# Kernel optimization log

Measured on AMD Instinct MI355X. Metric: run time of the kernel, lower is better.

## Reference

```python
import jax, jax.numpy as jnp
import numpy as np

N_HEADS = 8

def setup_inputs() -> dict:
    key = jax.random.key(0)
    ks = jax.random.split(key, 7)
    B, S, D = 4, 2048, 512
    s = 1.0 / np.sqrt(D)
    return {
        "input_Q": jax.random.normal(ks[0], (B, S, D), jnp.float32),
        "input_K": jax.random.normal(ks[1], (B, S, D), jnp.float32),
        "input_V": jax.random.normal(ks[2], (B, S, D), jnp.float32),
        "W_Q": jax.random.normal(ks[3], (D, D), jnp.float32) * s,
        "W_K": jax.random.normal(ks[4], (D, D), jnp.float32) * s,
        "W_V": jax.random.normal(ks[5], (D, D), jnp.float32) * s,
        "W_O": jax.random.normal(ks[6], (D, D), jnp.float32) * s,
    }

def reference(input_Q, input_K, input_V, W_Q, W_K, W_V, W_O):
    B, Sq, D = input_Q.shape
    Sk = input_K.shape[1]
    H = N_HEADS
    d_k = D // H
    # torch nn.Linear(bias=False): y = x @ W.T
    def proj(x, W):
        return (x @ W.T).reshape(B, -1, H, d_k).transpose(0, 2, 1, 3)  # [B,H,S,dk]
    Q = proj(input_Q, W_Q)
    K = proj(input_K, W_K)
    V = proj(input_V, W_V)
    scale = 1.0 / jnp.sqrt(jnp.float32(d_k))
    scores = jnp.einsum("bhqd,bhkd->bhqk", Q, K) * scale  # [B,H,Sq,Sk]
    # TriangularCausalMask: mask strict upper triangle with -inf
    causal = jnp.tril(jnp.ones((Sq, Sk), dtype=bool))
    scores = jnp.where(causal[None, None], scores, -jnp.inf)
    attn = jax.nn.softmax(scores, axis=-1)
    context = jnp.einsum("bhqk,bhkd->bhqd", attn, V)
    context = context.transpose(0, 2, 1, 3).reshape(B, Sq, D)
    return context @ W_O.T
```

## Files before the change

### kernel.cpp

```cpp
#include <hip/hip_runtime.h>
#include <hip/hip_bf16.h>
#include <math.h>

#define B_  4
#define S_  2048
#define D_  512
#define H_  8
#define DK_ 64
#define M_  (B_ * S_)

using bf16   = __bf16;
using bf16x4 = __bf16 __attribute__((ext_vector_type(4)));
using bf16x8 = __bf16 __attribute__((ext_vector_type(8)));
using f32x4  = float __attribute__((ext_vector_type(4)));

#define MFMA16(a, b, c) __builtin_amdgcn_mfma_f32_16x16x32_bf16((a), (b), (c), 0, 0, 0)
#define EXP2(x) exp2f(x)

typedef __attribute__((address_space(3))) void       lds_void;
typedef const __attribute__((address_space(1))) void gbl_void;

__device__ __forceinline__ void async16(const bf16* g, bf16* lds) {
    __builtin_amdgcn_global_load_lds((gbl_void*)g, (lds_void*)lds, 16, 0, 0);
}

__device__ __forceinline__ bf16x8 ldg8(const bf16* p) {
    return *reinterpret_cast<const bf16x8*>(p);
}

__device__ __forceinline__ size_t fragbase(int g, int k0, int kk, int t) {
    return ((((size_t)(g * 8 + k0) * 2 + kk) * 4 + t) * 64) * 8;
}

__global__ __launch_bounds__(256) void cvt_all(
    const float* __restrict__ x0, const float* __restrict__ x1, const float* __restrict__ x2,
    const float* __restrict__ w0, const float* __restrict__ w1,
    const float* __restrict__ w2, const float* __restrict__ w3,
    bf16* __restrict__ dst)
{
    const int w    = blockIdx.x * 4 + (threadIdx.x >> 6);
    const int lane = threadIdx.x & 63;
    const int lg = lane >> 4, lc = lane & 15;
    const float* src;
    int c;
    size_t dbase;
    if (w < 24576) {
        const int seg = w >> 13;
        c = w & 8191;
        src = (seg == 0) ? x0 : (seg == 1) ? x1 : x2;
        dbase = (size_t)seg << 22;
    } else {
        const int jj = w - 24576;
        const int seg = jj >> 9;
        c = jj & 511;
        src = (seg == 0) ? w0 : (seg == 1) ? w1 : (seg == 2) ? w2 : w3;
        dbase = ((size_t)3 << 22) + ((size_t)seg << 18);
    }
    const int g = c >> 6, k0 = (c >> 3) & 7, kk = (c >> 2) & 1, t = c & 3;
    const size_t soff = ((size_t)(g * 64 + t * 16 + lc) << 9) + k0 * 64 + kk * 32 + lg * 8;
    f32x4 a = *reinterpret_cast<const f32x4*>(src + soff);
    f32x4 b = *reinterpret_cast<const f32x4*>(src + soff + 4);
    bf16x8 r;
    #pragma unroll
    for (int j = 0; j < 4; ++j) { r[j] = (bf16)a[j]; r[j + 4] = (bf16)b[j]; }
    *reinterpret_cast<bf16x8*>(dst + dbase + ((size_t)c << 9) + (size_t)lane * 8) = r;
}

__global__ __launch_bounds__(256) void gemm_qkv(
    const bf16* __restrict__ Xf, const bf16* __restrict__ Wf,
    bf16* __restrict__ qkv)
{
    const int bx  = blockIdx.x;
    const int xcd = bx & 7;
    const int idx = bx >> 3;
    const int mt  = xcd + 8 * (idx & 7);
    const int rest = idx >> 3;
    const int nt  = rest & 3;
    const int z   = rest >> 2;

    const bf16* Xz = Xf + (size_t)z * M_ * D_;
    const bf16* Wz = Wf + (size_t)z * D_ * D_;
    const bool vz = (z == 2);
    const bf16* A  = vz ? Xz : Wz;
    const bf16* Bm = vz ? Wz : Xz;

    const int lane = threadIdx.x & 63;
    const int wave = threadIdx.x >> 6;
    const int lc = lane & 15;
    const int lg = lane >> 4;
    const int gA = (vz ? 2 * mt : 2 * nt) + (wave >> 1);
    const int gB = (vz ? 2 * nt : 2 * mt) + (wave & 1);

    f32x4 acc[4][4] = {};

    #pragma unroll
    for (int k0 = 0; k0 < 8; ++k0) {
        #pragma unroll
        for (int kk = 0; kk < 2; ++kk) {
            bf16x8 af[4], bfm[4];
            #pragma unroll
            for (int t = 0; t < 4; ++t)
                af[t] = ldg8(A + fragbase(gA, k0, kk, t) + (size_t)lane * 8);
            #pragma unroll
            for (int t = 0; t < 4; ++t)
                bfm[t] = ldg8(Bm + fragbase(gB, k0, kk, t) + (size_t)lane * 8);
            #pragma unroll
            for (int mi = 0; mi < 4; ++mi)
                #pragma unroll
                for (int ni = 0; ni < 4; ++ni)
                    acc[mi][ni] = MFMA16(af[mi], bfm[ni], acc[mi][ni]);
        }
    }

    if (z < 2) {
        bf16* Y = qkv + (size_t)z * M_ * D_;
        const float sc = (z == 0) ? 0.125f * 1.4426950408889634f : 1.0f;
        #pragma unroll
        for (int mi = 0; mi < 4; ++mi)
            #pragma unroll
            for (int ni = 0; ni < 4; ++ni) {
                const int d = gA * 64 + mi * 16 + lg * 4;
                const int s = gB * 64 + ni * 16 + lc;
                bf16x4 v;
                #pragma unroll
                for (int r = 0; r < 4; ++r) v[r] = (bf16)(acc[mi][ni][r] * sc);
                const size_t oidx =
                    ((((size_t)(s >> 11) * H_ + (d >> 6)) * S_
                      + (s & (S_ - 1))) << 6) + (d & 63);
                *reinterpret_cast<bf16x4*>(&Y[oidx]) = v;
            }
    } else {
        bf16* Y = qkv + (size_t)2 * M_ * D_;
        #pragma unroll
        for (int mi = 0; mi < 4; ++mi)
            #pragma unroll
            for (int ni = 0; ni < 4; ++ni) {
                const int s = gA * 64 + mi * 16 + lg * 4;
                const int d = gB * 64 + ni * 16 + lc;
                bf16x4 v;
                #pragma unroll
                for (int r = 0; r < 4; ++r) v[r] = (bf16)acc[mi][ni][r];
                const size_t oidx =
                    ((((size_t)(s >> 11)) * H_ + (d >> 6)) << 17)
                    + (size_t)(d & 63) * S_ + (s & (S_ - 1));
                *reinterpret_cast<bf16x4*>(&Y[oidx]) = v;
            }
    }
}

__global__ __launch_bounds__(256) void gemm_out(
    const bf16* __restrict__ CtxF, const bf16* __restrict__ WoF,
    float* __restrict__ out)
{
    const int bx  = blockIdx.x;
    const int xcd = bx & 7;
    const int idx = bx >> 3;
    const int mt  = xcd + 8 * (idx & 15);
    const int nt  = idx >> 4;

    const int lane = threadIdx.x & 63;
    const int wave = threadIdx.x >> 6;
    const int lc = lane & 15;
    const int lg = lane >> 4;
    const int gA = 2 * nt + (wave >> 1);
    const int tA = (wave & 1) * 2;
    const int gB = mt;

    f32x4 acc[2][4] = {};

    #pragma unroll
    for (int k0 = 0; k0 < 8; ++k0) {
        #pragma unroll
        for (int kk = 0; kk < 2; ++kk) {
            bf16x8 af[2], bfm[4];
            #pragma unroll
            for (int ai = 0; ai < 2; ++ai)
                af[ai] = ldg8(WoF + fragbase(gA, k0, kk, tA + ai) + (size_t)lane * 8);
            #pragma unroll
            for (int t = 0; t < 4; ++t)
                bfm[t] = ldg8(CtxF + fragbase(gB, k0, kk, t) + (size_t)lane * 8);
            #pragma unroll
            for (int ai = 0; ai < 2; ++ai)
                #pragma unroll
                for (int ni = 0; ni < 4; ++ni)
                    acc[ai][ni] = MFMA16(af[ai], bfm[ni], acc[ai][ni]);
        }
    }

    #pragma unroll
    for (int ai = 0; ai < 2; ++ai)
        #pragma unroll
        for (int ni = 0; ni < 4; ++ni) {
            const int d = gA * 64 + (tA + ai) * 16 + lg * 4;
            const int s = gB * 64 + ni * 16 + lc;
            *reinterpret_cast<f32x4*>(&out[(size_t)s * D_ + d]) = acc[ai][ni];
        }
}

__device__ __forceinline__ bf16x8 pfrag(const f32x4 a, const f32x4 b) {
    union U4 { bf16x4 v; unsigned int u[2]; };
    U4 pa, pb;
    #pragma unroll
    for (int r = 0; r < 4; ++r) { pa.v[r] = (bf16)a[r]; pb.v[r] = (bf16)b[r]; }
    auto r0 = __builtin_amdgcn_permlane16_swap(pa.u[0], pb.u[0], false, false);
    auto r1 = __builtin_amdgcn_permlane16_swap(pa.u[1], pb.u[1], false, false);
    union U8 { unsigned int u[4]; bf16x8 v; } out;
    out.u[0] = r0[0]; out.u[1] = r1[0]; out.u[2] = r0[1]; out.u[3] = r1[1];
    return out.v;
}

__global__ __launch_bounds__(512, 4) void attn(
    const bf16* __restrict__ QKV, bf16* __restrict__ CtxF)
{
    const int bx = blockIdx.x;
    const int bh = (bx & 7) * 4 + ((bx >> 3) & 3);
    const int pi = bx >> 5;
    const int b = bh >> 3, h = bh & 7;
    const size_t plane = (size_t)S_ * DK_;
    const bf16* Q  = QKV + (size_t)bh * plane;
    const bf16* Kp = QKV + (size_t)(B_ * H_) * plane + (size_t)bh * plane;
    const bf16* Vt = QKV + 2 * (size_t)(B_ * H_) * plane + (size_t)bh * plane;

    const int lane = threadIdx.x & 63;
    const int wave = threadIdx.x >> 6;
    const int wv   = wave & 3;
    const int half = wave >> 2;
    const int lc = lane & 15;
    const int lg = lane >> 4;
    const int sg = ((lg & 1) << 1) | (lg >> 1);
    const int srow = wv * 16 + lc;
    const int mrow = wv * 16 + lc;

    __shared__ bf16 Ks[4][64 * 64];
    __shared__ bf16 Vs[4][64 * 64];

    const int lo = pi;
    const int hi = 31 - pi;
    const int myq = half ? lo : hi;

    const int qR = myq * 64 + mrow;
    bf16x8 qf0 = ldg8(Q + (size_t)qR * DK_ + lg * 8);
    bf16x8 qf1 = ldg8(Q + (size_t)qR * DK_ + 32 + lg * 8);

    f32x4 accO[4] = {};
    float li = 0.f;

    auto stage = [&](int n) {
        const int kn = n * 64;
        if (half == 0) {
            bf16* kd = Ks[n & 3];
            #pragma unroll
            for (int i = 0; i < 2; ++i) {
                const int kc = i * 4 + lg;
                async16(Kp + (size_t)(kn + srow) * DK_ + kc * 8,
                        kd + (i * 256 + wv * 64) * 8);
            }
        } else {
            bf16* vd = Vs[n & 3];
            #pragma unroll
            for (int i = 0; i < 2; ++i) {
                const int kcv = i * 4 + sg;
                async16(Vt + (size_t)srow * S_ + kn + kcv * 8,
                        vd + (i * 256 + wv * 64) * 8);
            }
        }
    };

    stage(0); stage(1); stage(2);

    for (int j = 0; j <= hi; ++j) {
        if (j + 2 <= hi)      asm volatile("s_waitcnt vmcnt(4)" ::: "memory");
        else if (j + 1 <= hi) asm volatile("s_waitcnt vmcnt(2)" ::: "memory");
        else                  asm volatile("s_waitcnt vmcnt(0)" ::: "memory");
        __builtin_amdgcn_s_barrier();
        if (j + 3 <= hi) stage(j + 3);

        if (j <= myq) {
            const bf16* ks = Ks[j & 3];
            const bf16* vs = Vs[j & 3];

            bf16x8 kf0[4], kf1[4], vf0[4], vf1[4];
            #pragma unroll
            for (int t = 0; t < 4; ++t) {
                kf0[t] = ldg8(&ks[(t * 64 + lane) * 8]);
                kf1[t] = ldg8(&ks[(256 + t * 64 + lane) * 8]);
                vf0[t] = ldg8(&vs[(t * 64 + lane) * 8]);
                vf1[t] = ldg8(&vs[(256 + t * 64 + lane) * 8]);
            }

            f32x4 st[4];
            #pragma unroll
            for (int t = 0; t < 4; ++t) {
                f32x4 zz = {};
                zz = MFMA16(kf0[t], qf0, zz);
                st[t] = MFMA16(kf1[t], qf1, zz);
            }
            float rs = 0.f;
            if (j == myq) {
                #pragma unroll
                for (int t = 0; t < 4; ++t)
                    #pragma unroll
                    for (int r = 0; r < 4; ++r) {
                        const int kl = t * 16 + lg * 4 + r;
                        const float pv = EXP2((kl <= mrow) ? st[t][r] : -1e30f);
                        st[t][r] = pv;
                        rs += pv;
                    }
            } else {
                #pragma unroll
                for (int t = 0; t < 4; ++t)
                    #pragma unroll
                    for (int r = 0; r < 4; ++r) {
                        const float pv = EXP2(st[t][r]);
                        st[t][r] = pv;
                        rs += pv;
                    }
            }
            li += rs;

            const bf16x8 p0 = pfrag(st[0], st[1]);
            const bf16x8 p1 = pfrag(st[2], st[3]);

            #pragma unroll
            for (int t = 0; t < 4; ++t) {
                accO[t] = MFMA16(vf0[t], p0, accO[t]);
                accO[t] = MFMA16(vf1[t], p1, accO[t]);
            }
        }
    }

    li += __shfl_xor(li, 16); li += __shfl_xor(li, 32);
    const float rl = 1.0f / li;
    __syncthreads();
    bf16* T = &Ks[0][0] + wave * 1280;

    #pragma unroll
    for (int t = 0; t < 4; ++t) {
        bf16x4 ov;
        #pragma unroll
        for (int r = 0; r < 4; ++r) ov[r] = (bf16)(accO[t][r] * rl);
        *reinterpret_cast<bf16x4*>(&T[lc * 72 + t * 16 + lg * 4]) = ov;
    }
    #pragma unroll
    for (int kk = 0; kk < 2; ++kk) {
        bf16x8 o8 = ldg8(&T[lc * 72 + kk * 32 + lg * 8]);
        *reinterpret_cast<bf16x8*>(
            &CtxF[fragbase(b * 32 + myq, h, kk, wv) + (size_t)lane * 8]) = o8;
    }
}

extern "C" void kernel_launch(void* const* d_in, const int* in_sizes, int n_in,
                              void* d_out, int out_size, void* d_ws, size_t ws_size,
                              hipStream_t stream)
{
    float* out = (float*)d_out;

    bf16* Xf   = (bf16*)d_ws;
    bf16* Wf   = Xf + (size_t)3 * M_ * D_;
    bf16* qkv  = Wf + (size_t)4 * D_ * D_;
    bf16* ctxF = qkv + (size_t)3 * M_ * D_;

    cvt_all<<<6656, 256, 0, stream>>>(
        (const float*)d_in[0], (const float*)d_in[1], (const float*)d_in[2],
        (const float*)d_in[3], (const float*)d_in[4], (const float*)d_in[5],
        (const float*)d_in[6], Xf);

    gemm_qkv<<<dim3(768), 256, 0, stream>>>(Xf, Wf, qkv);
    attn<<<dim3(512), 512, 0, stream>>>(qkv, ctxF);
    gemm_out<<<dim3(512), 256, 0, stream>>>(ctxF, Wf + (size_t)3 * D_ * D_, out);
}
```

Before: 174.7 us.

## Stage GEMM operand fragments through triple-buffered LDS via async global-to-LDS loads

Result: no change. 174.8 us (+0.1%).

```diff
diff --git a/kernel.cpp b/kernel.cpp
--- a/kernel.cpp
+++ b/kernel.cpp
@@ -88,28 +88,55 @@
     const int wave = threadIdx.x >> 6;
     const int lc = lane & 15;
     const int lg = lane >> 4;
-    const int gA = (vz ? 2 * mt : 2 * nt) + (wave >> 1);
-    const int gB = (vz ? 2 * nt : 2 * mt) + (wave & 1);
+    const int gAb = vz ? 2 * mt : 2 * nt;
+    const int gBb = vz ? 2 * nt : 2 * mt;
+    const int aIdx = wave >> 1;
+    const int bIdx = wave & 1;
+    const int gA = gAb + aIdx;
+    const int gB = gBb + bIdx;
+
+    __shared__ bf16 Ab[3][4096];
+    __shared__ bf16 Bb[3][4096];
+
+    auto stage = [&](int s) {
+        const int k0 = s >> 1, kk = s & 1;
+        bf16* ad = Ab[s % 3];
+        bf16* bd = Bb[s % 3];
+        #pragma unroll
+        for (int i = 0; i < 4; ++i) {
+            const int c  = wave * 4 + i;
+            const int gx = (c >> 2) & 1;
+            const int t  = c & 3;
+            const bf16* srcb = (c < 8) ? A + fragbase(gAb + gx, k0, kk, t)
+                                       : Bm + fragbase(gBb + gx, k0, kk, t);
+            bf16* dstb = ((c < 8) ? ad : bd) + (gx * 4 + t) * 512;
+            async16(srcb + (size_t)lane * 8, dstb + (size_t)lane * 8);
+        }
+    };
 
     f32x4 acc[4][4] = {};
 
-    #pragma unroll
-    for (int k0 = 0; k0 < 8; ++k0) {
-        #pragma unroll
-        for (int kk = 0; kk < 2; ++kk) {
-            bf16x8 af[4], bfm[4];
-            #pragma unroll
-            for (int t = 0; t < 4; ++t)
-                af[t] = ldg8(A + fragbase(gA, k0, kk, t) + (size_t)lane * 8);
-            #pragma unroll
-            for (int t = 0; t < 4; ++t)
-                bfm[t] = ldg8(Bm + fragbase(gB, k0, kk, t) + (size_t)lane * 8);
-            #pragma unroll
-            for (int mi = 0; mi < 4; ++mi)
-                #pragma unroll
-                for (int ni = 0; ni < 4; ++ni)
-                    acc[mi][ni] = MFMA16(af[mi], bfm[ni], acc[mi][ni]);
-        }
+    stage(0); stage(1);
+
+    for (int s = 0; s < 16; ++s) {
+        if (s + 1 < 16) asm volatile("s_waitcnt vmcnt(4)" ::: "memory");
+        else            asm volatile("s_waitcnt vmcnt(0)" ::: "memory");
+        __builtin_amdgcn_s_barrier();
+        if (s + 2 < 16) stage(s + 2);
+
+        const bf16* ab = Ab[s % 3] + aIdx * 2048;
+        const bf16* bb = Bb[s % 3] + bIdx * 2048;
+        bf16x8 af[4], bfm[4];
+        #pragma unroll
+        for (int t = 0; t < 4; ++t) {
+            af[t]  = ldg8(ab + t * 512 + (size_t)lane * 8);
+            bfm[t] = ldg8(bb + t * 512 + (size_t)lane * 8);
+        }
+        #pragma unroll
+        for (int mi = 0; mi < 4; ++mi)
+            #pragma unroll
+            for (int ni = 0; ni < 4; ++ni)
+                acc[mi][ni] = MFMA16(af[mi], bfm[ni], acc[mi][ni]);
     }
 
     if (z < 2) {
@@ -166,25 +193,52 @@
     const int tA = (wave & 1) * 2;
     const int gB = mt;
 
+    __shared__ bf16 Ab[3][4096];
+    __shared__ bf16 Bb[3][2048];
+
+    auto stage = [&](int s) {
+        const int k0 = s >> 1, kk = s & 1;
+        bf16* ad = Ab[s % 3];
+        bf16* bd = Bb[s % 3];
+        #pragma unroll
+        for (int i = 0; i < 3; ++i) {
+            const int c = wave * 3 + i;
+            if (c < 8) {
+                const int gx = c >> 2, t = c & 3;
+                async16(WoF + fragbase(2 * nt + gx, k0, kk, t) + (size_t)lane * 8,
+                        ad + (gx * 4 + t) * 512 + (size_t)lane * 8);
+            } else {
+                const int t = c - 8;
+                async16(CtxF + fragbase(gB, k0, kk, t) + (size_t)lane * 8,
+                        bd + t * 512 + (size_t)lane * 8);
+            }
+        }
+    };
+
     f32x4 acc[2][4] = {};
 
-    #pragma unroll
-    for (int k0 = 0; k0 < 8; ++k0) {
-        #pragma unroll
-        for (int kk = 0; kk < 2; ++kk) {
-            bf16x8 af[2], bfm[4];
-            #pragma unroll
-            for (int ai = 0; ai < 2; ++ai)
-                af[ai] = ldg8(WoF + fragbase(gA, k0, kk, tA + ai) + (size_t)lane * 8);
-            #pragma unroll
-            for (int t = 0; t < 4; ++t)
-                bfm[t] = ldg8(CtxF + fragbase(gB, k0, kk, t) + (size_t)lane * 8);
-            #pragma unroll
-            for (int ai = 0; ai < 2; ++ai)
-                #pragma unroll
-                for (int ni = 0; ni < 4; ++ni)
-                    acc[ai][ni] = MFMA16(af[ai], bfm[ni], acc[ai][ni]);
-        }
+    stage(0); stage(1);
+
+    for (int s = 0; s < 16; ++s) {
+        if (s + 1 < 16) asm volatile("s_waitcnt vmcnt(3)" ::: "memory");
+        else            asm volatile("s_waitcnt vmcnt(0)" ::: "memory");
+        __builtin_amdgcn_s_barrier();
+        if (s + 2 < 16) stage(s + 2);
+
+        const bf16* ab = Ab[s % 3] + (wave >> 1) * 2048;
+        const bf16* bb = Bb[s % 3];
+        bf16x8 af[2], bfm[4];
+        #pragma unroll
+        for (int ai = 0; ai < 2; ++ai)
+            af[ai] = ldg8(ab + (tA + ai) * 512 + (size_t)lane * 8);
+        #pragma unroll
+        for (int t = 0; t < 4; ++t)
+            bfm[t] = ldg8(bb + t * 512 + (size_t)lane * 8);
+        #pragma unroll
+        for (int ai = 0; ai < 2; ++ai)
+            #pragma unroll
+            for (int ni = 0; ni < 4; ++ni)
+                acc[ai][ni] = MFMA16(af[ai], bfm[ni], acc[ai][ni]);
     }
 
     #pragma unroll
```

## Fuse four kernels into two using software grid barriers

Applied to the files above, without the earlier changes.

After: 348.6 us. +99.6%, slower.

```diff
diff --git a/kernel.cpp b/kernel.cpp
--- a/kernel.cpp
+++ b/kernel.cpp
@@ -32,44 +32,72 @@
     return ((((size_t)(g * 8 + k0) * 2 + kk) * 4 + t) * 64) * 8;
 }
 
-__global__ __launch_bounds__(256) void cvt_all(
-    const float* __restrict__ x0, const float* __restrict__ x1, const float* __restrict__ x2,
-    const float* __restrict__ w0, const float* __restrict__ w1,
-    const float* __restrict__ w2, const float* __restrict__ w3,
-    bf16* __restrict__ dst)
+__device__ __forceinline__ void gridbar(unsigned long long* cnt, unsigned G) {
+    __syncthreads();
+    if (threadIdx.x == 0) {
+        __threadfence();
+        unsigned long long v = __hip_atomic_fetch_add(
+            cnt, 1ULL, __ATOMIC_ACQ_REL, __HIP_MEMORY_SCOPE_AGENT);
+        const unsigned long long target = (v / G + 1) * G;
+        while (__hip_atomic_load(cnt, __ATOMIC_ACQUIRE,
+                                 __HIP_MEMORY_SCOPE_AGENT) < target)
+            __builtin_amdgcn_s_sleep(8);
+        __threadfence();
+    }
+    __syncthreads();
+}
+
+__global__ __launch_bounds__(256, 3) void k1_cvt_qkv(
+    const float* __restrict__ x0, const float* __restrict__ x1,
+    const float* __restrict__ x2, const float* __restrict__ w0,
+    const float* __restrict__ w1, const float* __restrict__ w2,
+    const float* __restrict__ w3, bf16* __restrict__ dst,
+    bf16* __restrict__ qkv, unsigned long long* bar)
 {
-    const int w    = blockIdx.x * 4 + (threadIdx.x >> 6);
     const int lane = threadIdx.x & 63;
-    const int lg = lane >> 4, lc = lane & 15;
-    const float* src;
-    int c;
-    size_t dbase;
-    if (w < 24576) {
-        const int seg = w >> 13;
-        c = w & 8191;
-        src = (seg == 0) ? x0 : (seg == 1) ? x1 : x2;
-        dbase = (size_t)seg << 22;
-    } else {
-        const int jj = w - 24576;
-        const int seg = jj >> 9;
-        c = jj & 511;
-        src = (seg == 0) ? w0 : (seg == 1) ? w1 : (seg == 2) ? w2 : w3;
-        dbase = ((size_t)3 << 22) + ((size_t)seg << 18);
-    }
-    const int g = c >> 6, k0 = (c >> 3) & 7, kk = (c >> 2) & 1, t = c & 3;
-    const size_t soff = ((size_t)(g * 64 + t * 16 + lc) << 9) + k0 * 64 + kk * 32 + lg * 8;
-    f32x4 a = *reinterpret_cast<const f32x4*>(src + soff);
-    f32x4 b = *reinterpret_cast<const f32x4*>(src + soff + 4);
-    bf16x8 r;
-    #pragma unroll
-    for (int j = 0; j < 4; ++j) { r[j] = (bf16)a[j]; r[j + 4] = (bf16)b[j]; }
-    *reinterpret_cast<bf16x8*>(dst + dbase + ((size_t)c << 9) + (size_t)lane * 8) = r;
-}
-
-__global__ __launch_bounds__(256) void gemm_qkv(
-    const bf16* __restrict__ Xf, const bf16* __restrict__ Wf,
-    bf16* __restrict__ qkv)
-{
+    const int wv   = threadIdx.x >> 6;
+    const int lc = lane & 15;
+    const int lg = lane >> 4;
+
+    {
+        const int gw = blockIdx.x * 4 + wv;
+        #pragma unroll
+        for (int i = 0; i < 9; ++i) {
+            const int cw = gw + 3072 * i;
+            if (cw >= 26624) break;
+            const float* src;
+            int c;
+            size_t dbase;
+            if (cw < 24576) {
+                const int seg = cw >> 13;
+                c = cw & 8191;
+                src = (seg == 0) ? x0 : (seg == 1) ? x1 : x2;
+                dbase = (size_t)seg << 22;
+            } else {
+                const int jj = cw - 24576;
+                const int seg = jj >> 9;
+                c = jj & 511;
+                src = (seg == 0) ? w0 : (seg == 1) ? w1 : (seg == 2) ? w2 : w3;
+                dbase = ((size_t)3 << 22) + ((size_t)seg << 18);
+            }
+            const int g = c >> 6, k0 = (c >> 3) & 7, kk = (c >> 2) & 1, t = c & 3;
+            const size_t soff = ((size_t)(g * 64 + t * 16 + lc) << 9)
+                                + k0 * 64 + kk * 32 + lg * 8;
+            f32x4 a = *reinterpret_cast<const f32x4*>(src + soff);
+            f32x4 b = *reinterpret_cast<const f32x4*>(src + soff + 4);
+            bf16x8 r;
+            #pragma unroll
+            for (int j = 0; j < 4; ++j) { r[j] = (bf16)a[j]; r[j + 4] = (bf16)b[j]; }
+            *reinterpret_cast<bf16x8*>(dst + dbase + ((size_t)c << 9)
+                                       + (size_t)lane * 8) = r;
+        }
+    }
+
+    gridbar(bar, 768);
+
+    const bf16* Xf = dst;
+    const bf16* Wf = dst + (size_t)3 * M_ * D_;
+
     const int bx  = blockIdx.x;
     const int xcd = bx & 7;
     const int idx = bx >> 3;
@@ -84,12 +112,8 @@
     const bf16* A  = vz ? Xz : Wz;
     const bf16* Bm = vz ? Wz : Xz;
 
-    const int lane = threadIdx.x & 63;
-    const int wave = threadIdx.x >> 6;
-    const int lc = lane & 15;
-    const int lg = lane >> 4;
-    const int gA = (vz ? 2 * mt : 2 * nt) + (wave >> 1);
-    const int gB = (vz ? 2 * nt : 2 * mt) + (wave & 1);
+    const int gA = (vz ? 2 * mt : 2 * nt) + (wv >> 1);
+    const int gB = (vz ? 2 * nt : 2 * mt) + (wv & 1);
 
     f32x4 acc[4][4] = {};
 
@@ -146,55 +170,6 @@
                 *reinterpret_cast<bf16x4*>(&Y[oidx]) = v;
             }
     }
-}
-
-__global__ __launch_bounds__(256) void gemm_out(
-    const bf16* __restrict__ CtxF, const bf16* __restrict__ WoF,
-    float* __restrict__ out)
-{
-    const int bx  = blockIdx.x;
-    const int xcd = bx & 7;
-    const int idx = bx >> 3;
-    const int mt  = xcd + 8 * (idx & 15);
-    const int nt  = idx >> 4;
-
-    const int lane = threadIdx.x & 63;
-    const int wave = threadIdx.x >> 6;
-    const int lc = lane & 15;
-    const int lg = lane >> 4;
-    const int gA = 2 * nt + (wave >> 1);
-    const int tA = (wave & 1) * 2;
-    const int gB = mt;
-
-    f32x4 acc[2][4] = {};
-
-    #pragma unroll
-    for (int k0 = 0; k0 < 8; ++k0) {
-        #pragma unroll
-        for (int kk = 0; kk < 2; ++kk) {
-            bf16x8 af[2], bfm[4];
-            #pragma unroll
-            for (int ai = 0; ai < 2; ++ai)
-                af[ai] = ldg8(WoF + fragbase(gA, k0, kk, tA + ai) + (size_t)lane * 8);
-            #pragma unroll
-            for (int t = 0; t < 4; ++t)
-                bfm[t] = ldg8(CtxF + fragbase(gB, k0, kk, t) + (size_t)lane * 8);
-            #pragma unroll
-            for (int ai = 0; ai < 2; ++ai)
-                #pragma unroll
-                for (int ni = 0; ni < 4; ++ni)
-                    acc[ai][ni] = MFMA16(af[ai], bfm[ni], acc[ai][ni]);
-        }
-    }
-
-    #pragma unroll
-    for (int ai = 0; ai < 2; ++ai)
-        #pragma unroll
-        for (int ni = 0; ni < 4; ++ni) {
-            const int d = gA * 64 + (tA + ai) * 16 + lg * 4;
-            const int s = gB * 64 + ni * 16 + lc;
-            *reinterpret_cast<f32x4*>(&out[(size_t)s * D_ + d]) = acc[ai][ni];
-        }
 }
 
 __device__ __forceinline__ bf16x8 pfrag(const f32x4 a, const f32x4 b) {
@@ -209,143 +184,183 @@
     return out.v;
 }
 
-__global__ __launch_bounds__(512, 4) void attn(
-    const bf16* __restrict__ QKV, bf16* __restrict__ CtxF)
+__global__ __launch_bounds__(512, 4) void k2_attn_out(
+    const bf16* __restrict__ QKV, bf16* __restrict__ CtxF,
+    const bf16* __restrict__ WoF, float* __restrict__ out,
+    unsigned long long* bar)
 {
     const int bx = blockIdx.x;
-    const int bh = (bx & 7) * 4 + ((bx >> 3) & 3);
-    const int pi = bx >> 5;
-    const int b = bh >> 3, h = bh & 7;
-    const size_t plane = (size_t)S_ * DK_;
-    const bf16* Q  = QKV + (size_t)bh * plane;
-    const bf16* Kp = QKV + (size_t)(B_ * H_) * plane + (size_t)bh * plane;
-    const bf16* Vt = QKV + 2 * (size_t)(B_ * H_) * plane + (size_t)bh * plane;
-
     const int lane = threadIdx.x & 63;
     const int wave = threadIdx.x >> 6;
-    const int wv   = wave & 3;
-    const int half = wave >> 2;
     const int lc = lane & 15;
     const int lg = lane >> 4;
-    const int sg = ((lg & 1) << 1) | (lg >> 1);
-    const int srow = wv * 16 + lc;
-    const int mrow = wv * 16 + lc;
 
     __shared__ bf16 Ks[4][64 * 64];
     __shared__ bf16 Vs[4][64 * 64];
 
-    const int lo = pi;
-    const int hi = 31 - pi;
-    const int myq = half ? lo : hi;
-
-    const int qR = myq * 64 + mrow;
-    bf16x8 qf0 = ldg8(Q + (size_t)qR * DK_ + lg * 8);
-    bf16x8 qf1 = ldg8(Q + (size_t)qR * DK_ + 32 + lg * 8);
-
-    f32x4 accO[4] = {};
-    float li = 0.f;
-
-    auto stage = [&](int n) {
-        const int kn = n * 64;
-        if (half == 0) {
-            bf16* kd = Ks[n & 3];
-            #pragma unroll
-            for (int i = 0; i < 2; ++i) {
-                const int kc = i * 4 + lg;
-                async16(Kp + (size_t)(kn + srow) * DK_ + kc * 8,
-                        kd + (i * 256 + wv * 64) * 8);
-            }
-        } else {
-            bf16* vd = Vs[n & 3];
-            #pragma unroll
-            for (int i = 0; i < 2; ++i) {
-                const int kcv = i * 4 + sg;
-                async16(Vt + (size_t)srow * S_ + kn + kcv * 8,
-                        vd + (i * 256 + wv * 64) * 8);
-            }
-        }
-    };
-
-    stage(0); stage(1); stage(2);
-
-    for (int j = 0; j <= hi; ++j) {
-        if (j + 2 <= hi)      asm volatile("s_waitcnt vmcnt(4)" ::: "memory");
-        else if (j + 1 <= hi) asm volatile("s_waitcnt vmcnt(2)" ::: "memory");
-        else                  asm volatile("s_waitcnt vmcnt(0)" ::: "memory");
-        __builtin_amdgcn_s_barrier();
-        if (j + 3 <= hi) stage(j + 3);
-
-        if (j <= myq) {
-            const bf16* ks = Ks[j & 3];
-            const bf16* vs = Vs[j & 3];
-
-            bf16x8 kf0[4], kf1[4], vf0[4], vf1[4];
-            #pragma unroll
-            for (int t = 0; t < 4; ++t) {
-                kf0[t] = ldg8(&ks[(t * 64 + lane) * 8]);
-                kf1[t] = ldg8(&ks[(256 + t * 64 + lane) * 8]);
-                vf0[t] = ldg8(&vs[(t * 64 + lane) * 8]);
-                vf1[t] = ldg8(&vs[(256 + t * 64 + lane) * 8]);
-            }
-
-            f32x4 st[4];
-            #pragma unroll
-            for (int t = 0; t < 4; ++t) {
-                f32x4 zz = {};
-                zz = MFMA16(kf0[t], qf0, zz);
-                st[t] = MFMA16(kf1[t], qf1, zz);
-            }
-            float rs = 0.f;
-            if (j == myq) {
+    {
+        const int bh = (bx & 7) * 4 + ((bx >> 3) & 3);
+        const int pi = bx >> 5;
+        const int b = bh >> 3, h = bh & 7;
+        const size_t plane = (size_t)S_ * DK_;
+        const bf16* Q  = QKV + (size_t)bh * plane;
+        const bf16* Kp = QKV + (size_t)(B_ * H_) * plane + (size_t)bh * plane;
+        const bf16* Vt = QKV + 2 * (size_t)(B_ * H_) * plane + (size_t)bh * plane;
+
+        const int wv   = wave & 3;
+        const int half = wave >> 2;
+        const int sg = ((lg & 1) << 1) | (lg >> 1);
+        const int srow = wv * 16 + lc;
+        const int mrow = wv * 16 + lc;
+
+        const int lo = pi;
+        const int hi = 31 - pi;
+        const int myq = half ? lo : hi;
+
+        const int qR = myq * 64 + mrow;
+        bf16x8 qf0 = ldg8(Q + (size_t)qR * DK_ + lg * 8);
+        bf16x8 qf1 = ldg8(Q + (size_t)qR * DK_ + 32 + lg * 8);
+
+        f32x4 accO[4] = {};
+        float li = 0.f;
+
+        auto stage = [&](int n) {
+            const int kn = n * 64;
+            if (half == 0) {
+                bf16* kd = Ks[n & 3];
+                #pragma unroll
+                for (int i = 0; i < 2; ++i) {
+                    const int kc = i * 4 + lg;
+                    async16(Kp + (size_t)(kn + srow) * DK_ + kc * 8,
+                            kd + (i * 256 + wv * 64) * 8);
+                }
+            } else {
+                bf16* vd = Vs[n & 3];
+                #pragma unroll
+                for (int i = 0; i < 2; ++i) {
+                    const int kcv = i * 4 + sg;
+                    async16(Vt + (size_t)srow * S_ + kn + kcv * 8,
+                            vd + (i * 256 + wv * 64) * 8);
+                }
+            }
+        };
+
+        stage(0); stage(1); stage(2);
+
+        for (int j = 0; j <= hi; ++j) {
+            if (j + 2 <= hi)      asm volatile("s_waitcnt vmcnt(4)" ::: "memory");
+            else if (j + 1 <= hi) asm volatile("s_waitcnt vmcnt(2)" ::: "memory");
+            else                  asm volatile("s_waitcnt vmcnt(0)" ::: "memory");
+            __builtin_amdgcn_s_barrier();
+            if (j + 3 <= hi) stage(j + 3);
+
+            if (j <= myq) {
+                const bf16* ks = Ks[j & 3];
+                const bf16* vs = Vs[j & 3];
+
+                bf16x8 kf0[4], kf1[4], vf0[4], vf1[4];
+                #pragma unroll
+                for (int t = 0; t < 4; ++t) {
+                    kf0[t] = ldg8(&ks[(t * 64 + lane) * 8]);
+                    kf1[t] = ldg8(&ks[(256 + t * 64 + lane) * 8]);
+                    vf0[t] = ldg8(&vs[(t * 64 + lane) * 8]);
+                    vf1[t] = ldg8(&vs[(256 + t * 64 + lane) * 8]);
+                }
+
+                f32x4 st[4];
+                #pragma unroll
+                for (int t = 0; t < 4; ++t) {
+                    f32x4 zz = {};
+                    zz = MFMA16(kf0[t], qf0, zz);
+                    st[t] = MFMA16(kf1[t], qf1, zz);
+                }
+                float rs = 0.f;
+                if (j == myq) {
+                    #pragma unroll
+                    for (int t = 0; t < 4; ++t)
+                        #pragma unroll
+                        for (int r = 0; r < 4; ++r) {
+                            const int kl = t * 16 + lg * 4 + r;
+                            const float pv = EXP2((kl <= mrow) ? st[t][r] : -1e30f);
+                            st[t][r] = pv;
+                            rs += pv;
+                        }
+                } else {
+                    #pragma unroll
+                    for (int t = 0; t < 4; ++t)
+                        #pragma unroll
+                        for (int r = 0; r < 4; ++r) {
+                            const float pv = EXP2(st[t][r]);
+                            st[t][r] = pv;
+                            rs += pv;
+                        }
+                }
+                li += rs;
+
+                const bf16x8 p0 = pfrag(st[0], st[1]);
+                const bf16x8 p1 = pfrag(st[2], st[3]);
+
+                #pragma unroll
+                for (int t = 0; t < 4; ++t) {
+                    accO[t] = MFMA16(vf0[t], p0, accO[t]);
+                    accO[t] = MFMA16(vf1[t], p1, accO[t]);
+                }
+            }
+        }
+
+        li += __shfl_xor(li, 16); li += __shfl_xor(li, 32);
+        const float rl = 1.0f / li;
+        __syncthreads();
+        bf16* T = &Ks[0][0] + wave * 1280;
+
+        #pragma unroll
+        for (int t = 0; t < 4; ++t) {
+            bf16x4 ov;
+            #pragma unroll
+            for (int r = 0; r < 4; ++r) ov[r] = (bf16)(accO[t][r] * rl);
+            *reinterpret_cast<bf16x4*>(&T[lc * 72 + t * 16 + lg * 4]) = ov;
+        }
+        #pragma unroll
+        for (int kk = 0; kk < 2; ++kk) {
+            bf16x8 o8 = ldg8(&T[lc * 72 + kk * 32 + lg * 8]);
+            *reinterpret_cast<bf16x8*>(
+                &CtxF[fragbase(b * 32 + myq, h, kk, wv) + (size_t)lane * 8]) = o8;
+        }
+    }
+
+    gridbar(bar, 512);
+
+    {
+        const int xcd = bx & 7;
+        const int idx = bx >> 3;
+        const int mt  = xcd + 8 * (idx & 15);
+        const int nt  = idx >> 4;
+        const int gA = 2 * nt + (wave >> 2);
+        const int tA = wave & 3;
+
+        f32x4 acc2[4] = {};
+
+        #pragma unroll
+        for (int k0 = 0; k0 < 8; ++k0) {
+            #pragma unroll
+            for (int kk = 0; kk < 2; ++kk) {
+                bf16x8 af = ldg8(WoF + fragbase(gA, k0, kk, tA) + (size_t)lane * 8);
+                bf16x8 bfm[4];
                 #pragma unroll
                 for (int t = 0; t < 4; ++t)
-                    #pragma unroll
-                    for (int r = 0; r < 4; ++r) {
-                        const int kl = t * 16 + lg * 4 + r;
-                        const float pv = EXP2((kl <= mrow) ? st[t][r] : -1e30f);
-                        st[t][r] = pv;
-                        rs += pv;
-                    }
-            } else {
-                #pragma unroll
-                for (int t = 0; t < 4; ++t)
-                    #pragma unroll
-                    for (int r = 0; r < 4; ++r) {
-                        const float pv = EXP2(st[t][r]);
-                        st[t][r] = pv;
-                        rs += pv;
-                    }
-            }
-            li += rs;
-
-            const bf16x8 p0 = pfrag(st[0], st[1]);
-            const bf16x8 p1 = pfrag(st[2], st[3]);
-
-            #pragma unroll
-            for (int t = 0; t < 4; ++t) {
-                accO[t] = MFMA16(vf0[t], p0, accO[t]);
-                accO[t] = MFMA16(vf1[t], p1, accO[t]);
-            }
-        }
-    }
-
-    li += __shfl_xor(li, 16); li += __shfl_xor(li, 32);
-    const float rl = 1.0f / li;
-    __syncthreads();
-    bf16* T = &Ks[0][0] + wave * 1280;
-
-    #pragma unroll
-    for (int t = 0; t < 4; ++t) {
-        bf16x4 ov;
-        #pragma unroll
-        for (int r = 0; r < 4; ++r) ov[r] = (bf16)(accO[t][r] * rl);
-        *reinterpret_cast<bf16x4*>(&T[lc * 72 + t * 16 + lg * 4]) = ov;
-    }
-    #pragma unroll
-    for (int kk = 0; kk < 2; ++kk) {
-        bf16x8 o8 = ldg8(&T[lc * 72 + kk * 32 + lg * 8]);
-        *reinterpret_cast<bf16x8*>(
-            &CtxF[fragbase(b * 32 + myq, h, kk, wv) + (size_t)lane * 8]) = o8;
+                    bfm[t] = ldg8(CtxF + fragbase(mt, k0, kk, t) + (size_t)lane * 8);
+                #pragma unroll
+                for (int ni = 0; ni < 4; ++ni)
+                    acc2[ni] = MFMA16(af, bfm[ni], acc2[ni]);
+            }
+        }
+
+        #pragma unroll
+        for (int ni = 0; ni < 4; ++ni) {
+            const int d = gA * 64 + tA * 16 + lg * 4;
+            const int s = mt * 64 + ni * 16 + lc;
+            *reinterpret_cast<f32x4*>(&out[(size_t)s * D_ + d]) = acc2[ni];
+        }
     }
 }
 
@@ -355,17 +370,20 @@
 {
     float* out = (float*)d_out;
 
-    bf16* Xf   = (bf16*)d_ws;
-    bf16* Wf   = Xf + (size_t)3 * M_ * D_;
+    bf16* dst  = (bf16*)d_ws;
+    bf16* Wf   = dst + (size_t)3 * M_ * D_;
     bf16* qkv  = Wf + (size_t)4 * D_ * D_;
     bf16* ctxF = qkv + (size_t)3 * M_ * D_;
-
-    cvt_all<<<6656, 256, 0, stream>>>(
+    unsigned long long* bars =
+        (unsigned long long*)(ctxF + (size_t)M_ * D_);
+
+    hipMemsetAsync(bars, 0, 64, stream);
+
+    k1_cvt_qkv<<<dim3(768), 256, 0, stream>>>(
         (const float*)d_in[0], (const float*)d_in[1], (const float*)d_in[2],
         (const float*)d_in[3], (const float*)d_in[4], (const float*)d_in[5],
-        (const float*)d_in[6], Xf);
-
-    gemm_qkv<<<dim3(768), 256, 0, stream>>>(Xf, Wf, qkv);
-    attn<<<dim3(512), 512, 0, stream>>>(qkv, ctxF);
-    gemm_out<<<dim3(512), 256, 0, stream>>>(ctxF, Wf + (size_t)3 * D_ * D_, out);
-}
+        (const float*)d_in[6], dst, qkv, bars);
+
+    k2_attn_out<<<dim3(512), 512, 0, stream>>>(
+        qkv, ctxF, Wf + (size_t)3 * D_ * D_, out, bars + 1);
+}
```

## Split attention key tiles across wave halves instead of pairing query tiles

Applied to the files above, without the earlier changes.

Result: slower. 182.8 us (+4.6%).

```diff
diff --git a/kernel.cpp b/kernel.cpp
--- a/kernel.cpp
+++ b/kernel.cpp
@@ -214,7 +214,7 @@
 {
     const int bx = blockIdx.x;
     const int bh = (bx & 7) * 4 + ((bx >> 3) & 3);
-    const int pi = bx >> 5;
+    const int q  = 31 - (bx >> 5);
     const int b = bh >> 3, h = bh & 7;
     const size_t plane = (size_t)S_ * DK_;
     const bf16* Q  = QKV + (size_t)bh * plane;
@@ -224,128 +224,128 @@
     const int lane = threadIdx.x & 63;
     const int wave = threadIdx.x >> 6;
     const int wv   = wave & 3;
-    const int half = wave >> 2;
+    const int kh   = wave >> 2;
     const int lc = lane & 15;
     const int lg = lane >> 4;
     const int sg = ((lg & 1) << 1) | (lg >> 1);
-    const int srow = wv * 16 + lc;
     const int mrow = wv * 16 + lc;
 
     __shared__ bf16 Ks[4][64 * 64];
     __shared__ bf16 Vs[4][64 * 64];
 
-    const int lo = pi;
-    const int hi = 31 - pi;
-    const int myq = half ? lo : hi;
-
-    const int qR = myq * 64 + mrow;
+    const int qR = q * 64 + mrow;
     bf16x8 qf0 = ldg8(Q + (size_t)qR * DK_ + lg * 8);
     bf16x8 qf1 = ldg8(Q + (size_t)qR * DK_ + 32 + lg * 8);
 
     f32x4 accO[4] = {};
     float li = 0.f;
 
+    const int srow = (wave & 3) * 16 + lc;
+    const int kc   = (wave >> 2) * 4 + lg;
+    const int kcv  = (wave >> 2) * 4 + sg;
     auto stage = [&](int n) {
         const int kn = n * 64;
-        if (half == 0) {
-            bf16* kd = Ks[n & 3];
-            #pragma unroll
-            for (int i = 0; i < 2; ++i) {
-                const int kc = i * 4 + lg;
-                async16(Kp + (size_t)(kn + srow) * DK_ + kc * 8,
-                        kd + (i * 256 + wv * 64) * 8);
-            }
+        async16(Kp + (size_t)(kn + srow) * DK_ + kc * 8,
+                Ks[n & 3] + (wave * 64 + lane) * 8);
+        async16(Vt + (size_t)srow * S_ + kn + kcv * 8,
+                Vs[n & 3] + (wave * 64 + lane) * 8);
+    };
+
+    stage(0); stage(1); stage(2);
+
+    for (int j = 0; j <= q; ++j) {
+        if (j + 2 <= q)      asm volatile("s_waitcnt vmcnt(4)" ::: "memory");
+        else if (j + 1 <= q) asm volatile("s_waitcnt vmcnt(2)" ::: "memory");
+        else                 asm volatile("s_waitcnt vmcnt(0)" ::: "memory");
+        __builtin_amdgcn_s_barrier();
+        if (j + 3 <= q) stage(j + 3);
+
+        const bf16* ks = Ks[j & 3];
+        const bf16* vs = Vs[j & 3];
+
+        bf16x8 kf0[2], kf1[2], vf[4];
+        #pragma unroll
+        for (int tt = 0; tt < 2; ++tt) {
+            const int t = 2 * kh + tt;
+            kf0[tt] = ldg8(&ks[(t * 64 + lane) * 8]);
+            kf1[tt] = ldg8(&ks[(256 + t * 64 + lane) * 8]);
+        }
+        #pragma unroll
+        for (int t = 0; t < 4; ++t)
+            vf[t] = ldg8(&vs[(kh * 256 + t * 64 + lane) * 8]);
+
+        f32x4 st[2];
+        #pragma unroll
+        for (int tt = 0; tt < 2; ++tt) {
+            f32x4 zz = {};
+            zz = MFMA16(kf0[tt], qf0, zz);
+            st[tt] = MFMA16(kf1[tt], qf1, zz);
+        }
+        float rs = 0.f;
+        if (j == q) {
+            #pragma unroll
+            for (int tt = 0; tt < 2; ++tt)
+                #pragma unroll
+                for (int r = 0; r < 4; ++r) {
+                    const int kl = (2 * kh + tt) * 16 + lg * 4 + r;
+                    const float pv = EXP2((kl <= mrow) ? st[tt][r] : -1e30f);
+                    st[tt][r] = pv;
+                    rs += pv;
+                }
         } else {
-            bf16* vd = Vs[n & 3];
-            #pragma unroll
-            for (int i = 0; i < 2; ++i) {
-                const int kcv = i * 4 + sg;
-                async16(Vt + (size_t)srow * S_ + kn + kcv * 8,
-                        vd + (i * 256 + wv * 64) * 8);
-            }
-        }
-    };
-
-    stage(0); stage(1); stage(2);
-
-    for (int j = 0; j <= hi; ++j) {
-        if (j + 2 <= hi)      asm volatile("s_waitcnt vmcnt(4)" ::: "memory");
-        else if (j + 1 <= hi) asm volatile("s_waitcnt vmcnt(2)" ::: "memory");
-        else                  asm volatile("s_waitcnt vmcnt(0)" ::: "memory");
-        __builtin_amdgcn_s_barrier();
-        if (j + 3 <= hi) stage(j + 3);
-
-        if (j <= myq) {
-            const bf16* ks = Ks[j & 3];
-            const bf16* vs = Vs[j & 3];
-
-            bf16x8 kf0[4], kf1[4], vf0[4], vf1[4];
-            #pragma unroll
-            for (int t = 0; t < 4; ++t) {
-                kf0[t] = ldg8(&ks[(t * 64 + lane) * 8]);
-                kf1[t] = ldg8(&ks[(256 + t * 64 + lane) * 8]);
-                vf0[t] = ldg8(&vs[(t * 64 + lane) * 8]);
-                vf1[t] = ldg8(&vs[(256 + t * 64 + lane) * 8]);
-            }
-
-            f32x4 st[4];
-            #pragma unroll
-            for (int t = 0; t < 4; ++t) {
-                f32x4 zz = {};
-                zz = MFMA16(kf0[t], qf0, zz);
-                st[t] = MFMA16(kf1[t], qf1, zz);
-            }
-            float rs = 0.f;
-            if (j == myq) {
-                #pragma unroll
-                for (int t = 0; t < 4; ++t)
-                    #pragma unroll
-                    for (int r = 0; r < 4; ++r) {
-                        const int kl = t * 16 + lg * 4 + r;
-                        const float pv = EXP2((kl <= mrow) ? st[t][r] : -1e30f);
-                        st[t][r] = pv;
-                        rs += pv;
-                    }
-            } else {
-                #pragma unroll
-                for (int t = 0; t < 4; ++t)
-                    #pragma unroll
-                    for (int r = 0; r < 4; ++r) {
-                        const float pv = EXP2(st[t][r]);
-                        st[t][r] = pv;
-                        rs += pv;
-                    }
-            }
-            li += rs;
-
-            const bf16x8 p0 = pfrag(st[0], st[1]);
-            const bf16x8 p1 = pfrag(st[2], st[3]);
-
-            #pragma unroll
-            for (int t = 0; t < 4; ++t) {
-                accO[t] = MFMA16(vf0[t], p0, accO[t]);
-                accO[t] = MFMA16(vf1[t], p1, accO[t]);
-            }
-        }
-    }
-
-    li += __shfl_xor(li, 16); li += __shfl_xor(li, 32);
-    const float rl = 1.0f / li;
+            #pragma unroll
+            for (int tt = 0; tt < 2; ++tt)
+                #pragma unroll
+                for (int r = 0; r < 4; ++r) {
+                    const float pv = EXP2(st[tt][r]);
+                    st[tt][r] = pv;
+                    rs += pv;
+                }
+        }
+        li += rs;
+
+        const bf16x8 p = pfrag(st[0], st[1]);
+
+        #pragma unroll
+        for (int t = 0; t < 4; ++t)
+            accO[t] = MFMA16(vf[t], p, accO[t]);
+    }
+
     __syncthreads();
-    bf16* T = &Ks[0][0] + wave * 1280;
-
-    #pragma unroll
-    for (int t = 0; t < 4; ++t) {
-        bf16x4 ov;
-        #pragma unroll
-        for (int r = 0; r < 4; ++r) ov[r] = (bf16)(accO[t][r] * rl);
-        *reinterpret_cast<bf16x4*>(&T[lc * 72 + t * 16 + lg * 4]) = ov;
-    }
-    #pragma unroll
-    for (int kk = 0; kk < 2; ++kk) {
-        bf16x8 o8 = ldg8(&T[lc * 72 + kk * 32 + lg * 8]);
-        *reinterpret_cast<bf16x8*>(
-            &CtxF[fragbase(b * 32 + myq, h, kk, wv) + (size_t)lane * 8]) = o8;
+    float* scr = (float*)&Vs[0][0];
+    if (kh == 1) {
+        float* s = scr + ((size_t)(wv * 64 + lane)) * 17;
+        #pragma unroll
+        for (int t = 0; t < 4; ++t)
+            #pragma unroll
+            for (int r = 0; r < 4; ++r) s[t * 4 + r] = accO[t][r];
+        s[16] = li;
+    }
+    __syncthreads();
+    if (kh == 0) {
+        const float* s = scr + ((size_t)(wv * 64 + lane)) * 17;
+        #pragma unroll
+        for (int t = 0; t < 4; ++t)
+            #pragma unroll
+            for (int r = 0; r < 4; ++r) accO[t][r] += s[t * 4 + r];
+        li += s[16];
+        li += __shfl_xor(li, 16); li += __shfl_xor(li, 32);
+        const float rl = 1.0f / li;
+        bf16* T = &Ks[0][0] + wv * 1280;
+
+        #pragma unroll
+        for (int t = 0; t < 4; ++t) {
+            bf16x4 ov;
+            #pragma unroll
+            for (int r = 0; r < 4; ++r) ov[r] = (bf16)(accO[t][r] * rl);
+            *reinterpret_cast<bf16x4*>(&T[lc * 72 + t * 16 + lg * 4]) = ov;
+        }
+        #pragma unroll
+        for (int kk = 0; kk < 2; ++kk) {
+            bf16x8 o8 = ldg8(&T[lc * 72 + kk * 32 + lg * 8]);
+            *reinterpret_cast<bf16x8*>(
+                &CtxF[fragbase(b * 32 + q, h, kk, wv) + (size_t)lane * 8]) = o8;
+        }
     }
 }
 
@@ -366,6 +366,6 @@
         (const float*)d_in[6], Xf);
 
     gemm_qkv<<<dim3(768), 256, 0, stream>>>(Xf, Wf, qkv);
-    attn<<<dim3(512), 512, 0, stream>>>(qkv, ctxF);
+    attn<<<dim3(1024), 512, 0, stream>>>(qkv, ctxF);
     gemm_out<<<dim3(512), 256, 0, stream>>>(ctxF, Wf + (size_t)3 * D_ * D_, out);
 }
```
